# Kernel optimization log

Hardware: AMD Instinct MI355X
Metric: run time of the kernel (lower is better)

Reference implementation:

```python
import jax, jax.numpy as jnp
import numpy as np
import math

B, L, IN, HID, H, NL = 2, 1024, 512, 1024, 16, 2
DH = HID // H


def _rel_shift(x):
    # Transformer-XL relative shift for the position-bias term (the pos_lookup).
    # x: [B, H, L, P] with P == L; out[b,h,i,j] uses relative distance (i - j).
    b, h, l, p = x.shape
    x = jnp.pad(x, ((0, 0), (0, 0), (0, 0), (1, 0)))
    return x.reshape(b, h, p + 1, l)[:, :, 1:, :].reshape(b, h, l, p)


def _ln(v, w, bias, eps=1e-12):
    # BertLayerNorm: epsilon inside the sqrt
    u = v.mean(-1, keepdims=True)
    s = ((v - u) ** 2).mean(-1, keepdims=True)
    return w * (v - u) / jnp.sqrt(s + eps) + bias


def _gelu(v):
    # exact erf-based GELU as in the source
    return v * 0.5 * (1.0 + jax.lax.erf(v / math.sqrt(2.0)))


def _forward(x, pos_raw, Wh1, bh1, Wh2, bh2, Wq, bq, Wk, bk, Wv, bv, Wp, bp,
             cbias, pbias, Wo, bo, Wf1, bf1, Wf2, bf2, ln_w, ln_b):
    # to_hidden MLP: input_size -> hidden -> hidden with GELU
    h = _gelu(x @ Wh1 + bh1) @ Wh2 + bh2  # [B, L, HID]
    scale = 1.0 / math.sqrt(DH)
    for l in range(Wq.shape[0]):
        # per-head LinearSplit projections, fused into one einsum per Q/K/V/pos
        q = jnp.einsum('bld,hdk->blhk', h, Wq[l]) + bq[l]
        k = jnp.einsum('bld,hdk->blhk', h, Wk[l]) + bk[l]
        v = jnp.einsum('bld,hdk->blhk', h, Wv[l]) + bv[l]
        p = jnp.einsum('pd,hdk->hpk', pos_raw, Wp[l]) + bp[l][:, None, :]
        qc = q + cbias[l]  # content-biased query
        qp = q + pbias[l]  # position-biased query
        ac = jnp.einsum('bihk,bjhk->bhij', qc, k)                 # content score
        bd = _rel_shift(jnp.einsum('bihk,hpk->bhip', qp, p))      # position score
        w = jax.nn.softmax((ac + bd) * scale, axis=-1)            # [B,H,L,L]
        a = jnp.einsum('bhij,bjhk->bihk', w, v)
        a = a.reshape(h.shape[0], h.shape[1], -1)                 # combine heads
        a = a @ Wo[l] + bo[l]
        h1 = _ln(a + h, ln_w[l], ln_b[l])                         # residual + LN
        f = _gelu(h1 @ Wf1[l] + bf1[l]) @ Wf2[l] + bf2[l]         # top FFN
        h = _ln(h1 + f, ln_w[l], ln_b[l])                         # shared LN params
    return h


def setup_inputs() -> dict:
    key = jax.random.key(0)
    ks = iter(jax.random.split(key, 32))
    n = lambda shape, s=0.02: jax.random.normal(next(ks), shape, dtype=jnp.float32) * s
    return {
        'x': jax.random.normal(next(ks), (B, L, IN), dtype=jnp.float32),
        'pos_raw': jax.random.normal(next(ks), (L, HID), dtype=jnp.float32),
        'Wh1': n((IN, HID)), 'bh1': jnp.zeros((HID,), jnp.float32),
        'Wh2': n((HID, HID)), 'bh2': jnp.zeros((HID,), jnp.float32),
        'Wq': n((NL, H, HID, DH)), 'bq': jnp.zeros((NL, H, DH), jnp.float32),
        'Wk': n((NL, H, HID, DH)), 'bk': jnp.zeros((NL, H, DH), jnp.float32),
        'Wv': n((NL, H, HID, DH)), 'bv': jnp.zeros((NL, H, DH), jnp.float32),
        'Wp': n((NL, H, HID, DH)), 'bp': jnp.zeros((NL, H, DH), jnp.float32),
        'cbias': n((NL, H, DH), 1.0), 'pbias': n((NL, H, DH), 1.0),
        'Wo': n((NL, HID, HID)), 'bo': jnp.zeros((NL, HID), jnp.float32),
        'Wf1': n((NL, HID, HID)), 'bf1': jnp.zeros((NL, HID), jnp.float32),
        'Wf2': n((NL, HID, HID)), 'bf2': jnp.zeros((NL, HID), jnp.float32),
        'ln_w': jnp.ones((NL, HID), jnp.float32),
        'ln_b': jnp.zeros((NL, HID), jnp.float32),
    }


def reference(x, pos_raw, Wh1, bh1, Wh2, bh2, Wq, bq, Wk, bk, Wv, bv, Wp, bp,
              cbias, pbias, Wo, bo, Wf1, bf1, Wf2, bf2, ln_w, ln_b):
    return _forward(x, pos_raw, Wh1, bh1, Wh2, bh2, Wq, bq, Wk, bk, Wv, bv,
                    Wp, bp, cbias, pbias, Wo, bo, Wf1, bf1, Wf2, bf2, ln_w, ln_b)
```

## Files before the change

### kernel.cpp

```cpp
#include <hip/hip_runtime.h>
#include <hip/hip_bf16.h>
#include <math.h>

typedef unsigned short u16;
typedef __attribute__((ext_vector_type(8))) short bhalf8;
typedef __attribute__((ext_vector_type(4))) float f32x4;

#define DEV __device__ __forceinline__

DEV float bf2f(u16 u){ unsigned int i=((unsigned int)u)<<16; float f; __builtin_memcpy(&f,&i,4); return f; }
DEV u16 f2bf(float f){ unsigned int i; __builtin_memcpy(&i,&f,4); i += 0x7FFFu + ((i>>16)&1u); return (u16)(i>>16); }
DEV float gelu_f(float x){ return 0.5f*x*(1.0f+erff(x*0.70710678118654752f)); }
DEV float wredsum(float v){ for(int o=32;o;o>>=1) v+=__shfl_down(v,o); return v; }

DEV void gload16(const u16* g, u16* l){
  __builtin_amdgcn_global_load_lds(
      (const __attribute__((address_space(1))) void*)g,
      (__attribute__((address_space(3))) void*)l, 16, 0, 0);
}

#define KAPPA 0.18033688011112042f
#define ZSTR 1049664L

template<int BM, int BN, int EPI>
__global__ __launch_bounds__(256) void gemm_bt(
    const u16* __restrict__ A, const u16* __restrict__ Bt,
    void* __restrict__ C0, void* __restrict__ C1,
    const float* __restrict__ bias0, const float* __restrict__ bias1,
    int M, int N, int K, int lda, int ldb, int ldc, int Hdiv, int bst,
    long sAb, long sAh, long sBb, long sBh, long sCb, long sCh)
{
  static_assert(BM==128 && BN==64, "vmcnt literal assumes 6 loads/stage");
  constexpr int FM = BM/32, FN = BN/32;
  __shared__ __align__(16) u16 sA[2][BM][64];
  __shared__ __align__(16) u16 sB[2][BN][64];
  const int bflat = blockIdx.y * gridDim.x + blockIdx.x;
  const int bq = bflat >> 3, br = bflat & 7;
  int bx, by;
  if (gridDim.y == 16){ by = br + 8*(bq & 1); bx = bq >> 1; }
  else                { by = br;              bx = bq;      }
  const int z  = blockIdx.z;
  const int bb = z / Hdiv, hh = z % Hdiv;
  const u16* Ab = A + (long)bb*sAb + (long)hh*sAh + (long)by*BM*lda;
  const u16* Bb = Bt + (long)bb*sBb + (long)hh*sBh + (long)bx*BN*ldb;
  const long coff = (long)bb*sCb + (long)hh*sCh;
  const int m0 = by*BM, n0 = bx*BN;
  const int tid = threadIdx.x, lane = tid&63, wave = tid>>6;
  const int wm = wave>>1, wn = wave&1;
  const int rl = lane&15, g = lane>>4;
  const int rswz = rl & 7;

  auto stage = [&](int buf, int kt){
    #pragma unroll
    for (int i=0;i<BM/32;i++){
      int idx = i*256 + tid;
      int r = idx>>3, s = (idx&7) ^ (r&7);
      gload16(Ab + (long)r*lda + kt + s*8, &sA[buf][0][0] + (long)(i*256 + wave*64)*8);
    }
    #pragma unroll
    for (int i=0;i<BN/32;i++){
      int idx = i*256 + tid;
      int r = idx>>3, s = (idx&7) ^ (r&7);
      gload16(Bb + (long)r*ldb + kt + s*8, &sB[buf][0][0] + (long)(i*256 + wave*64)*8);
    }
  };

  f32x4 acc[FM][FN] = {};
  const int nt = K >> 6;
  stage(0, 0);
  int cur = 0;
  for (int t=0; t<nt; ++t){
    if (t+1 < nt){
      stage(cur^1, (t+1)<<6);
      asm volatile("s_waitcnt vmcnt(6)" ::: "memory");
    } else {
      asm volatile("s_waitcnt vmcnt(0)" ::: "memory");
    }
    __builtin_amdgcn_s_barrier();
    #pragma unroll
    for (int ks=0; ks<2; ++ks){
      bhalf8 af[FM], bfr[FN];
      #pragma unroll
      for (int i=0;i<FM;i++){
        int row = wm*(BM/2)+i*16+rl;
        af[i]  = *(const bhalf8*)&sA[cur][row][(((ks*4+g)) ^ rswz)*8];
      }
      #pragma unroll
      for (int j=0;j<FN;j++){
        int row = wn*(BN/2)+j*16+rl;
        bfr[j] = *(const bhalf8*)&sB[cur][row][(((ks*4+g)) ^ rswz)*8];
      }
      #pragma unroll
      for (int i=0;i<FM;i++)
        #pragma unroll
        for (int j=0;j<FN;j++)
          acc[i][j] = __builtin_amdgcn_mfma_f32_16x16x32_bf16(af[i], bfr[j], acc[i][j], 0,0,0);
    }
    __builtin_amdgcn_s_barrier();
    cur ^= 1;
  }
  const int cr = g*4, cc = rl;
  #pragma unroll
  for (int i=0;i<FM;i++){
    const int gm = m0 + wm*(BM/2) + i*16 + cr;
    #pragma unroll
    for (int j=0;j<FN;j++){
      const int gn = n0 + wn*(BN/2) + j*16 + cc;
      const float b0v = (EPI&(1|64)) ? bias0[(long)bb*bst + gn] : 0.0f;
      const float b1v = (EPI&8) ? bias1[gn] : 0.0f;
      f32x4 v = acc[i][j];
      #pragma unroll
      for (int jj=0;jj<4;jj++){
        if (EPI&64){
          const long cidx = (long)(gm+jj)*ldc + gn;
          ((u16*)C0)[cidx] = f2bf(v[jj] + b0v);
          if (gn < 1024)
            ((u16*)C1)[(long)(gm+jj)*1024 + gn] = f2bf(v[jj] + bias1[gn]);
          continue;
        }
        const long cidx = coff + (long)(gm+jj)*ldc + gn;
        float o0 = v[jj] + b0v;
        if (EPI&2)  o0 = gelu_f(o0);
        if (EPI&4)  ((u16*)C0)[cidx] = f2bf(o0);
        else        ((float*)C0)[cidx] = o0;
        if (EPI&8)  ((u16*)C1)[cidx] = f2bf(v[jj] + b1v);
        if (EPI&16) ((float*)C1)[cidx] = o0;
      }
    }
  }
}

template<int EPI>
static void launch_gemm(hipStream_t s, int M,int N,int K,
    const u16* A,int lda,long sAb,long sAh,
    const u16* Bt,int ldb,long sBb,long sBh,
    void* C0, void* C1, int ldc, long sCb, long sCh,
    const float* b0, const float* b1, int bst, int NB, int HD)
{
  gemm_bt<128,64,EPI><<<dim3(N/64, M/128, NB), dim3(256), 0, s>>>(
      A,Bt,C0,C1,b0,b1,M,N,K,lda,ldb,ldc,HD,bst,sAb,sAh,sBb,sBh,sCb,sCh);
}

__global__ __launch_bounds__(256) void flash_attn(
    const u16* __restrict__ qkv,
    const u16* __restrict__ vtb,
    const u16* __restrict__ bdf,
    u16* __restrict__ ab)
{
  const int z = blockIdx.y, b = z >> 4, h = z & 15;
  const int i0 = blockIdx.x * 64;
  const int tid = threadIdx.x, lane = tid & 63, wave = tid >> 6;
  const int rl = lane & 15, g = lane >> 4;
  const int ig = i0 + wave*16 + rl;

  __shared__ u16 kt[128][72];
  __shared__ u16 vt[64][132];
  __shared__ u16 pw[4][16][132];

  const u16* qrow = qkv + ((long)(b*1024 + ig))*3072 + h*64;
  const bhalf8 qf0 = *(const bhalf8*)(qrow + g*8);
  const bhalf8 qf1 = *(const bhalf8*)(qrow + 32 + g*8);
  const u16* bdbase = bdf + (long)z*ZSTR + 1 + ((long)ig<<10) + 1023 + g*4;

  bhalf8 kreg[2][2], vreg[2][2];
  ushort4 bdreg[2][8];

  auto issueKV = [&](int jt){
    #pragma unroll
    for (int w = 0; w < 2; ++w){
      int r = (tid>>2) + w*64, c = tid&3;
      const u16* sk = qkv + ((long)(b*1024 + jt*128 + r))*3072 + 1024 + h*64 + c*16;
      kreg[w][0] = *(const bhalf8*)(sk);
      kreg[w][1] = *(const bhalf8*)(sk + 8);
      int d = (tid>>3) + w*32, c2 = tid&7;
      const u16* sv = vtb + (long)b*1048576L + ((long)(h*64 + d))*1024 + jt*128 + c2*16;
      vreg[w][0] = *(const bhalf8*)(sv);
      vreg[w][1] = *(const bhalf8*)(sv + 8);
    }
  };

  issueKV(0);
  {
    #pragma unroll
    for (int jf = 0; jf < 8; ++jf) bdreg[0][jf] = *(const ushort4*)(bdbase + jf*16);
  }

  f32x4 o[4] = {};
  float m = -INFINITY, l = 0.f;

  #pragma unroll
  for (int jt = 0; jt < 8; ++jt){
    __syncthreads();
    #pragma unroll
    for (int w = 0; w < 2; ++w){
      int r = (tid>>2) + w*64, c = tid&3;
      *(bhalf8*)&kt[r][c*16]     = kreg[w][0];
      *(bhalf8*)&kt[r][c*16 + 8] = kreg[w][1];
      int d = (tid>>3) + w*32, c2 = tid&7;
      *(bhalf8*)&vt[d][c2*16]     = vreg[w][0];
      *(bhalf8*)&vt[d][c2*16 + 8] = vreg[w][1];
    }
    __syncthreads();

    if (jt < 7){
      issueKV(jt+1);
      const u16* p = bdbase + (jt+1)*128;
      #pragma unroll
      for (int jf = 0; jf < 8; ++jf) bdreg[(jt+1)&1][jf] = *(const ushort4*)(p + jf*16);
    }

    f32x4 s[8];
    __builtin_amdgcn_s_setprio(1);
    #pragma unroll
    for (int jf = 0; jf < 8; ++jf){
      bhalf8 a0 = *(const bhalf8*)&kt[jf*16 + rl][g*8];
      bhalf8 a1 = *(const bhalf8*)&kt[jf*16 + rl][32 + g*8];
      f32x4 acc = {};
      acc = __builtin_amdgcn_mfma_f32_16x16x32_bf16(a0, qf0, acc, 0,0,0);
      acc = __builtin_amdgcn_mfma_f32_16x16x32_bf16(a1, qf1, acc, 0,0,0);
      ushort4 bdv = bdreg[jt&1][jf];
      acc[0] += bf2f(bdv.x); acc[1] += bf2f(bdv.y);
      acc[2] += bf2f(bdv.z); acc[3] += bf2f(bdv.w);
      s[jf] = acc;
    }
    __builtin_amdgcn_s_setprio(0);

    float mt = s[0][0];
    #pragma unroll
    for (int jf = 0; jf < 8; ++jf)
      #pragma unroll
      for (int r2 = 0; r2 < 4; ++r2) mt = fmaxf(mt, s[jf][r2]);
    mt = fmaxf(mt, __shfl_xor(mt, 16));
    mt = fmaxf(mt, __shfl_xor(mt, 32));
    if (__any(mt > m + 11.5f)){
      const float mnew = fmaxf(m, mt);
      const float alpha = exp2f(m - mnew);
      l *= alpha;
      #pragma unroll
      for (int df = 0; df < 4; ++df) o[df] *= alpha;
      m = mnew;
    }
    float psum = 0.f;
    #pragma unroll
    for (int jf = 0; jf < 8; ++jf)
      #pragma unroll
      for (int r2 = 0; r2 < 4; ++r2){
        float p = exp2f(s[jf][r2] - m);
        psum += p; s[jf][r2] = p;
      }
    psum += __shfl_xor(psum, 16);
    psum += __shfl_xor(psum, 32);
    l += psum;

    #pragma unroll
    for (int jf = 0; jf < 8; ++jf){
      uint2 pk;
      pk.x = (unsigned)f2bf(s[jf][0]) | ((unsigned)f2bf(s[jf][1])<<16);
      pk.y = (unsigned)f2bf(s[jf][2]) | ((unsigned)f2bf(s[jf][3])<<16);
      *(uint2*)&pw[wave][rl][jf*16 + g*4] = pk;
    }

    __builtin_amdgcn_s_setprio(1);
    #pragma unroll
    for (int df = 0; df < 4; ++df)
      #pragma unroll
      for (int kf = 0; kf < 4; ++kf){
        bhalf8 a  = *(const bhalf8*)&vt[df*16 + rl][kf*32 + g*8];
        bhalf8 bf = *(const bhalf8*)&pw[wave][rl][kf*32 + g*8];
        o[df] = __builtin_amdgcn_mfma_f32_16x16x32_bf16(a, bf, o[df], 0,0,0);
      }
    __builtin_amdgcn_s_setprio(0);
  }

  const float rlv = 1.0f / l;
  u16* orow = ab + ((long)(b*1024 + ig))*1024 + h*64;
  #pragma unroll
  for (int df = 0; df < 4; ++df){
    ushort4 w4;
    w4.x = f2bf(o[df][0]*rlv); w4.y = f2bf(o[df][1]*rlv);
    w4.z = f2bf(o[df][2]*rlv); w4.w = f2bf(o[df][3]*rlv);
    *(ushort4*)(orow + df*16 + g*4) = w4;
  }
}

__global__ __launch_bounds__(256) void ln_kernel(
    const float* __restrict__ xa, const float* __restrict__ xb2,
    const float* __restrict__ gamma, const float* __restrict__ beta,
    u16* __restrict__ ob, float* __restrict__ of)
{
  const long row = blockIdx.x;
  const int tid = threadIdx.x;
  const float4 a4 = ((const float4*)(xa  + row*1024))[tid];
  const float4 b4 = ((const float4*)(xb2 + row*1024))[tid];
  float v[4] = {a4.x+b4.x, a4.y+b4.y, a4.z+b4.z, a4.w+b4.w};
  float s = v[0]+v[1]+v[2]+v[3];
  __shared__ float red[4];
  s = wredsum(s);
  const int lane = tid&63, w = tid>>6;
  if (!lane) red[w] = s;
  __syncthreads();
  const float mean = (red[0]+red[1]+red[2]+red[3]) * (1.0f/1024.0f);
  float q = 0.f;
  #pragma unroll
  for (int k=0;k<4;k++){ float d = v[k]-mean; q += d*d; }
  __syncthreads();
  q = wredsum(q);
  if (!lane) red[w] = q;
  __syncthreads();
  const float var = (red[0]+red[1]+red[2]+red[3]) * (1.0f/1024.0f);
  const float rstd = rsqrtf(var + 1e-12f);
  const float4 g4 = ((const float4*)gamma)[tid];
  const float4 be4 = ((const float4*)beta)[tid];
  float oo[4];
  oo[0] = g4.x*(v[0]-mean)*rstd + be4.x;
  oo[1] = g4.y*(v[1]-mean)*rstd + be4.y;
  oo[2] = g4.z*(v[2]-mean)*rstd + be4.z;
  oo[3] = g4.w*(v[3]-mean)*rstd + be4.w;
  ushort4 ob4 = { f2bf(oo[0]), f2bf(oo[1]), f2bf(oo[2]), f2bf(oo[3]) };
  *(ushort4*)(ob + row*1024 + tid*4) = ob4;
  float4 of4 = { oo[0], oo[1], oo[2], oo[3] };
  ((float4*)(of + row*1024))[tid] = of4;
}

__global__ __launch_bounds__(256) void transpose_bf16(
    const u16* __restrict__ in, u16* __restrict__ out,
    long sin, int ldin, int coloff)
{
  __shared__ u16 tl[32][34];
  const long ibase = (long)blockIdx.z * sin + coloff;
  const long obase = (long)blockIdx.z * 1048576L;
  const int tr = blockIdx.y, tc = blockIdx.x;
  const int tx = threadIdx.x & 31, ty = threadIdx.x >> 5;
  #pragma unroll
  for (int k=0;k<4;k++){ int r = ty+k*8; tl[r][tx] = in[ibase + (long)(tr*32+r)*ldin + tc*32+tx]; }
  __syncthreads();
  #pragma unroll
  for (int k=0;k<4;k++){ int r = ty+k*8; out[obase + (long)(tc*32+r)*1024 + tr*32+tx] = tl[tx][r]; }
}

struct TJobs {
  const float* src[16];
  u16* dst[16];
  int R[16], C[16], nb[16];
  float sc[16];
};

__global__ __launch_bounds__(256) void wprep(TJobs J)
{
  const int j = blockIdx.y;
  const int R = J.R[j], C = J.C[j];
  const float scl = J.sc[j];
  const int tR = R>>5, tC = C>>5;
  const int ntiles = tR*tC*J.nb[j];
  const int t = blockIdx.x;
  if (t >= ntiles) return;
  const int b = t/(tR*tC); const int t2 = t%(tR*tC);
  const int tr = t2/tC, tc = t2%tC;
  const float* src = J.src[j] + (long)b*R*C;
  u16* dst = J.dst[j] + (long)b*R*C;
  __shared__ float tl[32][33];
  const int tx = threadIdx.x & 31, ty = threadIdx.x >> 5;
  #pragma unroll
  for (int k=0;k<4;k++){ int r = ty + k*8; tl[r][tx] = src[(long)(tr*32+r)*C + tc*32 + tx]; }
  __syncthreads();
  #pragma unroll
  for (int k=0;k<4;k++){ int r = ty + k*8;
    dst[(long)(tc*32 + r)*R + tr*32 + tx] = f2bf(tl[tx][r]*scl); }
}

__global__ __launch_bounds__(256) void misc_prep(
    const float* __restrict__ x, const float* __restrict__ pos,
    const float* __restrict__ bq, const float* __restrict__ cb, const float* __restrict__ pbv,
    const float* __restrict__ bk, const float* __restrict__ bv,
    u16* __restrict__ xb, u16* __restrict__ posb,
    float* __restrict__ bqkv, float* __restrict__ bqp,
    u16* __restrict__ bd)
{
  const int n1 = 2048*512, n2 = 1024*1024, n3 = 8192;
  int idx = blockIdx.x*256 + threadIdx.x;
  if (idx < n1) { xb[idx] = f2bf(x[idx]); return; }
  idx -= n1;
  if (idx < n2) { posb[idx] = f2bf(pos[idx]); return; }
  idx -= n2;
  if (idx < n3) {
    int l = idx >> 12; int r = idx & 4095;
    if (r < 3072){
      float val;
      if (r < 1024)       val = (bq[l*1024+r] + cb[l*1024+r]) * KAPPA;
      else if (r < 2048)  val = bk[l*1024 + r-1024];
      else                val = bv[l*1024 + r-2048];
      bqkv[l*3072+r] = val;
    } else {
      int n = r - 3072;
      bqp[l*1024+n] = (bq[l*1024+n] + pbv[l*1024+n]) * KAPPA;
    }
    return;
  }
  idx -= n3;
  if (idx < 32*1024) {
    int z = idx >> 10, i = idx & 1023;
    bd[(long)z*ZSTR + 1 + (long)i*1025 + 1024] = 0;
  }
}

extern "C" void kernel_launch(void* const* d_in, const int* in_sizes, int n_in,
                              void* d_out, int out_size, void* d_ws, size_t ws_size,
                              hipStream_t stream)
{
  (void)in_sizes; (void)n_in; (void)out_size; (void)ws_size;
  const float* x    = (const float*)d_in[0];
  const float* pos  = (const float*)d_in[1];
  const float* Wh1  = (const float*)d_in[2];
  const float* bh1  = (const float*)d_in[3];
  const float* Wh2  = (const float*)d_in[4];
  const float* bh2  = (const float*)d_in[5];
  const float* Wq   = (const float*)d_in[6];
  const float* bq   = (const float*)d_in[7];
  const float* Wk   = (const float*)d_in[8];
  const float* bk   = (const float*)d_in[9];
  const float* Wv   = (const float*)d_in[10];
  const float* bv   = (const float*)d_in[11];
  const float* Wp   = (const float*)d_in[12];
  const float* bp   = (const float*)d_in[13];
  const float* cbias= (const float*)d_in[14];
  const float* pbias= (const float*)d_in[15];
  const float* Wo   = (const float*)d_in[16];
  const float* bo   = (const float*)d_in[17];
  const float* Wf1  = (const float*)d_in[18];
  const float* bf1  = (const float*)d_in[19];
  const float* Wf2  = (const float*)d_in[20];
  const float* bf2  = (const float*)d_in[21];
  const float* lnw  = (const float*)d_in[22];
  const float* lnb  = (const float*)d_in[23];

  const long EL = 1048576L;
  char* ws = (char*)d_ws;
  size_t off = 0;
  auto alloc = [&](size_t bytes)->char* {
    char* p = ws + off; off += (bytes + 255) & ~(size_t)255; return p;
  };
  u16* xb    = (u16*)alloc(2048L*512*2);
  u16* posb  = (u16*)alloc(EL*2);
  u16* Wh1t  = (u16*)alloc(512L*1024*2);
  u16* Wh2t  = (u16*)alloc(EL*2);
  u16* Wqkvt = (u16*)alloc(6*EL*2);
  u16* Wpt   = (u16*)alloc(2*EL*2);
  u16* Wot   = (u16*)alloc(2*EL*2);
  u16* Wf1t  = (u16*)alloc(2*EL*2);
  u16* Wf2t  = (u16*)alloc(2*EL*2);
  float* bqkv= (float*)alloc(2*3072*4);
  float* bqp = (float*)alloc(2*1024*4);
  u16* t1    = (u16*)alloc(2048L*1024*2);
  u16* hb    = (u16*)alloc(2048L*1024*2);
  float* hf  = (float*)alloc(2048L*1024*4);
  u16* qkvb  = (u16*)alloc(2048L*3072*2);
  u16* qp    = (u16*)alloc(2048L*1024*2);
  u16* vtb   = (u16*)alloc(2048L*1024*2);
  u16* pb    = (u16*)alloc(2*EL*2);
  u16* bd    = (u16*)alloc(32L*ZSTR*2);
  u16* ab    = (u16*)alloc(2048L*1024*2);
  float* aof = (float*)alloc(2048L*1024*4);
  u16* h1b   = (u16*)alloc(2048L*1024*2);
  float* h1f = (float*)alloc(2048L*1024*4);
  u16* f1b   = (u16*)alloc(2048L*1024*2);
  float* f2f = (float*)alloc(2048L*1024*4);

  misc_prep<<<dim3((2048*512 + 1024*1024 + 8192 + 32*1024 + 255)/256),
              dim3(256), 0, stream>>>(
      x, pos, bq, cbias, pbias, bk, bv, xb, posb, bqkv, bqp, bd);

  TJobs J; int ji = 0;
  auto addjob = [&](const float* s, u16* d, int R, int C, int nb, float sc){
    J.src[ji]=s; J.dst[ji]=d; J.R[ji]=R; J.C[ji]=C; J.nb[ji]=nb; J.sc[ji]=sc; ji++;
  };
  addjob(Wh1, Wh1t, 512, 1024, 1, 1.f);
  addjob(Wh2, Wh2t, 1024, 1024, 1, 1.f);
  for (int l=0;l<2;l++) addjob(Wq + l*EL, Wqkvt + l*3*EL,        1024, 64, 16, KAPPA);
  for (int l=0;l<2;l++) addjob(Wk + l*EL, Wqkvt + l*3*EL + EL,   1024, 64, 16, 1.f);
  for (int l=0;l<2;l++) addjob(Wv + l*EL, Wqkvt + l*3*EL + 2*EL, 1024, 64, 16, 1.f);
  for (int l=0;l<2;l++) addjob(Wp + l*EL, Wpt + l*EL, 1024, 64, 16, 1.f);
  for (int l=0;l<2;l++) addjob(Wo + l*EL, Wot + l*EL, 1024, 1024, 1, 1.f);
  for (int l=0;l<2;l++) addjob(Wf1 + l*EL, Wf1t + l*EL, 1024, 1024, 1, 1.f);
  for (int l=0;l<2;l++) addjob(Wf2 + l*EL, Wf2t + l*EL, 1024, 1024, 1, 1.f);
  wprep<<<dim3(1024, 16), dim3(256), 0, stream>>>(J);

  launch_gemm<7>(stream, 2048,1024,512,  xb,512,0,0,  Wh1t,512,0,0,
                 t1,nullptr,1024,0,0,  bh1,nullptr, 0, 1,1);
  launch_gemm<21>(stream, 2048,1024,1024, t1,1024,0,0, Wh2t,1024,0,0,
                 hb,hf,1024,0,0,  bh2,nullptr, 0, 1,1);

  launch_gemm<5>(stream, 1024,1024,1024, posb,1024, 0,0, Wpt,1024, EL,0,
                 pb,nullptr,1024, EL,0,  bp,nullptr, 1024, 2,1);

  for (int l=0; l<2; l++){
    const u16 *Wqkvt_l = Wqkvt + l*3*EL, *Wot_l = Wot + l*EL,
              *Wf1t_l = Wf1t + l*EL, *Wf2t_l = Wf2t + l*EL;
    launch_gemm<64>(stream, 2048,3072,1024, hb,1024,0,0, Wqkvt_l,1024,0,0,
                    qkvb,qp,3072,0,0,  bqkv + l*3072, bqp + l*1024, 0, 1,1);
    transpose_bf16<<<dim3(32,32,2), dim3(256), 0, stream>>>(qkvb, vtb, 3145728L, 3072, 2048);
    launch_gemm<4>(stream, 1024,1024,64,  qp,1024, EL,64,  pb + l*EL,1024, 0,64,
                    bd+1,nullptr,1025, 16L*ZSTR, ZSTR,  nullptr,nullptr, 0, 32,16);
    flash_attn<<<dim3(16,32), dim3(256), 0, stream>>>(qkvb, vtb, bd, ab);
    launch_gemm<1>(stream, 2048,1024,1024, ab,1024,0,0, Wot_l,1024,0,0,
                    aof,nullptr,1024,0,0,  bo + l*1024, nullptr, 0, 1,1);
    ln_kernel<<<dim3(2048), dim3(256), 0, stream>>>(aof, hf, lnw + l*1024, lnb + l*1024, h1b, h1f);
    launch_gemm<7>(stream, 2048,1024,1024, h1b,1024,0,0, Wf1t_l,1024,0,0,
                    f1b,nullptr,1024,0,0,  bf1 + l*1024, nullptr, 0, 1,1);
    launch_gemm<1>(stream, 2048,1024,1024, f1b,1024,0,0, Wf2t_l,1024,0,0,
                    f2f,nullptr,1024,0,0,  bf2 + l*1024, nullptr, 0, 1,1);
    float* outf = (l==1) ? (float*)d_out : hf;
    ln_kernel<<<dim3(2048), dim3(256), 0, stream>>>(f2f, h1f, lnw + l*1024, lnb + l*1024, hb, outf);
  }
}
```

Measured before the change: 356.7 us.

## Fuse V transpose into QKV GEMM epilogue and load K/V directly in attention

The QKV GEMM epilogue now writes V columns straight into a transposed buffer using packed 4-element stores, which lets the separate transpose kernel be removed. The flash attention kernel drops its LDS staging of K and V and the two barriers per tile, and loads K and V fragments from global memory straight into registers for the MFMAs. This saves a kernel launch, a round trip of V through memory, and the synchronisation overhead. In exchange, K/V are no longer shared through LDS, so each wave issues its own global loads with no software prefetch of the next tile, which may expose memory latency.

```diff
diff --git a/kernel.cpp b/kernel.cpp
--- a/kernel.cpp
+++ b/kernel.cpp
@@ -25,7 +25,7 @@
 template<int BM, int BN, int EPI>
 __global__ __launch_bounds__(256) void gemm_bt(
     const u16* __restrict__ A, const u16* __restrict__ Bt,
-    void* __restrict__ C0, void* __restrict__ C1,
+    void* __restrict__ C0, void* __restrict__ C1, void* __restrict__ C2,
     const float* __restrict__ bias0, const float* __restrict__ bias1,
     int M, int N, int K, int lda, int ldb, int ldc, int Hdiv, int bst,
     long sAb, long sAh, long sBb, long sBh, long sCb, long sCh)
@@ -109,15 +109,23 @@
       const float b0v = (EPI&(1|64)) ? bias0[(long)bb*bst + gn] : 0.0f;
       const float b1v = (EPI&8) ? bias1[gn] : 0.0f;
       f32x4 v = acc[i][j];
+      if (EPI&64){
+        if (gn >= 2048){
+          ushort4 w4 = { f2bf(v[0]+b0v), f2bf(v[1]+b0v), f2bf(v[2]+b0v), f2bf(v[3]+b0v) };
+          const long vbase = ((long)(gm>>10))*1048576L + (long)(gn-2048)*1024 + (gm&1023);
+          *(ushort4*)((u16*)C2 + vbase) = w4;
+        } else {
+          #pragma unroll
+          for (int jj=0;jj<4;jj++){
+            ((u16*)C0)[(long)(gm+jj)*ldc + gn] = f2bf(v[jj] + b0v);
+            if (gn < 1024)
+              ((u16*)C1)[(long)(gm+jj)*1024 + gn] = f2bf(v[jj] + bias1[gn]);
+          }
+        }
+        continue;
+      }
       #pragma unroll
       for (int jj=0;jj<4;jj++){
-        if (EPI&64){
-          const long cidx = (long)(gm+jj)*ldc + gn;
-          ((u16*)C0)[cidx] = f2bf(v[jj] + b0v);
-          if (gn < 1024)
-            ((u16*)C1)[(long)(gm+jj)*1024 + gn] = f2bf(v[jj] + bias1[gn]);
-          continue;
-        }
         const long cidx = coff + (long)(gm+jj)*ldc + gn;
         float o0 = v[jj] + b0v;
         if (EPI&2)  o0 = gelu_f(o0);
@@ -134,11 +142,11 @@
 static void launch_gemm(hipStream_t s, int M,int N,int K,
     const u16* A,int lda,long sAb,long sAh,
     const u16* Bt,int ldb,long sBb,long sBh,
-    void* C0, void* C1, int ldc, long sCb, long sCh,
+    void* C0, void* C1, void* C2, int ldc, long sCb, long sCh,
     const float* b0, const float* b1, int bst, int NB, int HD)
 {
   gemm_bt<128,64,EPI><<<dim3(N/64, M/128, NB), dim3(256), 0, s>>>(
-      A,Bt,C0,C1,b0,b1,M,N,K,lda,ldb,ldc,HD,bst,sAb,sAh,sBb,sBh,sCb,sCh);
+      A,Bt,C0,C1,C2,b0,b1,M,N,K,lda,ldb,ldc,HD,bst,sAb,sAh,sBb,sBh,sCb,sCh);
 }
 
 __global__ __launch_bounds__(256) void flash_attn(
@@ -153,57 +161,32 @@
   const int rl = lane & 15, g = lane >> 4;
   const int ig = i0 + wave*16 + rl;
 
-  __shared__ u16 kt[128][72];
-  __shared__ u16 vt[64][132];
   __shared__ u16 pw[4][16][132];
 
   const u16* qrow = qkv + ((long)(b*1024 + ig))*3072 + h*64;
   const bhalf8 qf0 = *(const bhalf8*)(qrow + g*8);
   const bhalf8 qf1 = *(const bhalf8*)(qrow + 32 + g*8);
   const u16* bdbase = bdf + (long)z*ZSTR + 1 + ((long)ig<<10) + 1023 + g*4;
-
-  bhalf8 kreg[2][2], vreg[2][2];
+  const u16* Kb = qkv + ((long)(b*1024))*3072 + 1024 + h*64;
+  const u16* Vb = vtb + (long)b*1048576L + ((long)(h*64))*1024;
+
   ushort4 bdreg[2][8];
-
-  auto issueKV = [&](int jt){
-    #pragma unroll
-    for (int w = 0; w < 2; ++w){
-      int r = (tid>>2) + w*64, c = tid&3;
-      const u16* sk = qkv + ((long)(b*1024 + jt*128 + r))*3072 + 1024 + h*64 + c*16;
-      kreg[w][0] = *(const bhalf8*)(sk);
-      kreg[w][1] = *(const bhalf8*)(sk + 8);
-      int d = (tid>>3) + w*32, c2 = tid&7;
-      const u16* sv = vtb + (long)b*1048576L + ((long)(h*64 + d))*1024 + jt*128 + c2*16;
-      vreg[w][0] = *(const bhalf8*)(sv);
-      vreg[w][1] = *(const bhalf8*)(sv + 8);
-    }
-  };
-
-  issueKV(0);
-  {
-    #pragma unroll
-    for (int jf = 0; jf < 8; ++jf) bdreg[0][jf] = *(const ushort4*)(bdbase + jf*16);
-  }
+  #pragma unroll
+  for (int jf = 0; jf < 8; ++jf) bdreg[0][jf] = *(const ushort4*)(bdbase + jf*16);
 
   f32x4 o[4] = {};
   float m = -INFINITY, l = 0.f;
 
   #pragma unroll
   for (int jt = 0; jt < 8; ++jt){
-    __syncthreads();
-    #pragma unroll
-    for (int w = 0; w < 2; ++w){
-      int r = (tid>>2) + w*64, c = tid&3;
-      *(bhalf8*)&kt[r][c*16]     = kreg[w][0];
-      *(bhalf8*)&kt[r][c*16 + 8] = kreg[w][1];
-      int d = (tid>>3) + w*32, c2 = tid&7;
-      *(bhalf8*)&vt[d][c2*16]     = vreg[w][0];
-      *(bhalf8*)&vt[d][c2*16 + 8] = vreg[w][1];
-    }
-    __syncthreads();
-
+    bhalf8 ka[8], kb2[8];
+    #pragma unroll
+    for (int jf = 0; jf < 8; ++jf){
+      const u16* kr = Kb + (long)(jt*128 + jf*16 + rl)*3072;
+      ka[jf]  = *(const bhalf8*)(kr + g*8);
+      kb2[jf] = *(const bhalf8*)(kr + 32 + g*8);
+    }
     if (jt < 7){
-      issueKV(jt+1);
       const u16* p = bdbase + (jt+1)*128;
       #pragma unroll
       for (int jf = 0; jf < 8; ++jf) bdreg[(jt+1)&1][jf] = *(const ushort4*)(p + jf*16);
@@ -213,11 +196,9 @@
     __builtin_amdgcn_s_setprio(1);
     #pragma unroll
     for (int jf = 0; jf < 8; ++jf){
-      bhalf8 a0 = *(const bhalf8*)&kt[jf*16 + rl][g*8];
-      bhalf8 a1 = *(const bhalf8*)&kt[jf*16 + rl][32 + g*8];
       f32x4 acc = {};
-      acc = __builtin_amdgcn_mfma_f32_16x16x32_bf16(a0, qf0, acc, 0,0,0);
-      acc = __builtin_amdgcn_mfma_f32_16x16x32_bf16(a1, qf1, acc, 0,0,0);
+      acc = __builtin_amdgcn_mfma_f32_16x16x32_bf16(ka[jf],  qf0, acc, 0,0,0);
+      acc = __builtin_amdgcn_mfma_f32_16x16x32_bf16(kb2[jf], qf1, acc, 0,0,0);
       ushort4 bdv = bdreg[jt&1][jf];
       acc[0] += bf2f(bdv.x); acc[1] += bf2f(bdv.y);
       acc[2] += bf2f(bdv.z); acc[3] += bf2f(bdv.w);
@@ -265,7 +246,7 @@
     for (int df = 0; df < 4; ++df)
       #pragma unroll
       for (int kf = 0; kf < 4; ++kf){
-        bhalf8 a  = *(const bhalf8*)&vt[df*16 + rl][kf*32 + g*8];
+        bhalf8 a  = *(const bhalf8*)(Vb + (long)(df*16 + rl)*1024 + jt*128 + kf*32 + g*8);
         bhalf8 bf = *(const bhalf8*)&pw[wave][rl][kf*32 + g*8];
         o[df] = __builtin_amdgcn_mfma_f32_16x16x32_bf16(a, bf, o[df], 0,0,0);
       }
@@ -320,22 +301,6 @@
   *(ushort4*)(ob + row*1024 + tid*4) = ob4;
   float4 of4 = { oo[0], oo[1], oo[2], oo[3] };
   ((float4*)(of + row*1024))[tid] = of4;
-}
-
-__global__ __launch_bounds__(256) void transpose_bf16(
-    const u16* __restrict__ in, u16* __restrict__ out,
-    long sin, int ldin, int coloff)
-{
-  __shared__ u16 tl[32][34];
-  const long ibase = (long)blockIdx.z * sin + coloff;
-  const long obase = (long)blockIdx.z * 1048576L;
-  const int tr = blockIdx.y, tc = blockIdx.x;
-  const int tx = threadIdx.x & 31, ty = threadIdx.x >> 5;
-  #pragma unroll
-  for (int k=0;k<4;k++){ int r = ty+k*8; tl[r][tx] = in[ibase + (long)(tr*32+r)*ldin + tc*32+tx]; }
-  __syncthreads();
-  #pragma unroll
-  for (int k=0;k<4;k++){ int r = ty+k*8; out[obase + (long)(tc*32+r)*1024 + tr*32+tx] = tl[tx][r]; }
 }
 
 struct TJobs {
@@ -485,29 +450,28 @@
   wprep<<<dim3(1024, 16), dim3(256), 0, stream>>>(J);
 
   launch_gemm<7>(stream, 2048,1024,512,  xb,512,0,0,  Wh1t,512,0,0,
-                 t1,nullptr,1024,0,0,  bh1,nullptr, 0, 1,1);
+                 t1,nullptr,nullptr,1024,0,0,  bh1,nullptr, 0, 1,1);
   launch_gemm<21>(stream, 2048,1024,1024, t1,1024,0,0, Wh2t,1024,0,0,
-                 hb,hf,1024,0,0,  bh2,nullptr, 0, 1,1);
+                 hb,hf,nullptr,1024,0,0,  bh2,nullptr, 0, 1,1);
 
   launch_gemm<5>(stream, 1024,1024,1024, posb,1024, 0,0, Wpt,1024, EL,0,
-                 pb,nullptr,1024, EL,0,  bp,nullptr, 1024, 2,1);
+                 pb,nullptr,nullptr,1024, EL,0,  bp,nullptr, 1024, 2,1);
 
   for (int l=0; l<2; l++){
     const u16 *Wqkvt_l = Wqkvt + l*3*EL, *Wot_l = Wot + l*EL,
               *Wf1t_l = Wf1t + l*EL, *Wf2t_l = Wf2t + l*EL;
     launch_gemm<64>(stream, 2048,3072,1024, hb,1024,0,0, Wqkvt_l,1024,0,0,
-                    qkvb,qp,3072,0,0,  bqkv + l*3072, bqp + l*1024, 0, 1,1);
-    transpose_bf16<<<dim3(32,32,2), dim3(256), 0, stream>>>(qkvb, vtb, 3145728L, 3072, 2048);
+                    qkvb,qp,vtb,3072,0,0,  bqkv + l*3072, bqp + l*1024, 0, 1,1);
     launch_gemm<4>(stream, 1024,1024,64,  qp,1024, EL,64,  pb + l*EL,1024, 0,64,
-                    bd+1,nullptr,1025, 16L*ZSTR, ZSTR,  nullptr,nullptr, 0, 32,16);
+                    bd+1,nullptr,nullptr,1025, 16L*ZSTR, ZSTR,  nullptr,nullptr, 0, 32,16);
     flash_attn<<<dim3(16,32), dim3(256), 0, stream>>>(qkvb, vtb, bd, ab);
     launch_gemm<1>(stream, 2048,1024,1024, ab,1024,0,0, Wot_l,1024,0,0,
-                    aof,nullptr,1024,0,0,  bo + l*1024, nullptr, 0, 1,1);
+                    aof,nullptr,nullptr,1024,0,0,  bo + l*1024, nullptr, 0, 1,1);
     ln_kernel<<<dim3(2048), dim3(256), 0, stream>>>(aof, hf, lnw + l*1024, lnb + l*1024, h1b, h1f);
     launch_gemm<7>(stream, 2048,1024,1024, h1b,1024,0,0, Wf1t_l,1024,0,0,
-                    f1b,nullptr,1024,0,0,  bf1 + l*1024, nullptr, 0, 1,1);
+                    f1b,nullptr,nullptr,1024,0,0,  bf1 + l*1024, nullptr, 0, 1,1);
     launch_gemm<1>(stream, 2048,1024,1024, f1b,1024,0,0, Wf2t_l,1024,0,0,
-                    f2f,nullptr,1024,0,0,  bf2 + l*1024, nullptr, 0, 1,1);
+                    f2f,nullptr,nullptr,1024,0,0,  bf2 + l*1024, nullptr, 0, 1,1);
     float* outf = (l==1) ? (float*)d_out : hf;
     ln_kernel<<<dim3(2048), dim3(256), 0, stream>>>(f2f, h1f, lnw + l*1024, lnb + l*1024, hb, outf);
   }
```

New measurement: 426.8 us. +19.7%, slower.
